# Kernel tuning notes

Hardware: AMD Instinct MI355X
Metric: run time of the kernel (lower is better)

Reference implementation:

```python
import jax, jax.numpy as jnp
import numpy as np

PATCH = 768
POS = 64
HID = 512
B, N = 8, 2048


def setup_inputs() -> dict:
    key = jax.random.key(0)
    ks = jax.random.split(key, 8)
    d_in = PATCH + POS
    s = 1.0 / np.sqrt(d_in)
    return {
        "patches": jax.random.normal(ks[0], (B, N, PATCH), jnp.float32),
        "positions": jax.random.normal(ks[1], (B, N, POS), jnp.float32),
        "Wq": jax.random.uniform(ks[2], (d_in, HID), jnp.float32, -s, s),
        "bq": jax.random.uniform(ks[3], (HID,), jnp.float32, -s, s),
        "Wk": jax.random.uniform(ks[4], (d_in, HID), jnp.float32, -s, s),
        "bk": jax.random.uniform(ks[5], (d_in and HID,), jnp.float32, -s, s),
        "Wv": jax.random.uniform(ks[6], (d_in, HID), jnp.float32, -s, s),
        "bv": jax.random.uniform(ks[7], (HID,), jnp.float32, -s, s),
    }


def reference(patches, positions, Wq, bq, Wk, bk, Wv, bv):
    # concat patch features with positional features: [B, N, PATCH+POS]
    x = jnp.concatenate([patches, positions], axis=-1)
    Q = x @ Wq + bq  # [B, N, HID]
    K = x @ Wk + bk
    V = x @ Wv + bv
    scale = jnp.sqrt(jnp.asarray(HID, x.dtype))
    scores = jnp.einsum("bnd,bmd->bnm", Q, K) / scale  # [B, N, N]
    weights = jax.nn.softmax(scores, axis=-1)
    return jnp.einsum("bnm,bmd->bnd", weights, V)  # [B, N, HID]
```

## Files before the change

kernel.cpp:

```cpp
#include <hip/hip_runtime.h>
#include <hip/hip_bf16.h>
#include <math.h>

typedef __hip_bfloat16 bf16;
typedef __attribute__((ext_vector_type(4))) float f32x4;
typedef __attribute__((ext_vector_type(8))) short s16x8;

typedef const __attribute__((address_space(1))) void gvoid_t;
typedef __attribute__((address_space(3))) void lvoid_t;

__device__ __forceinline__ void gload16(const void* g, void* l) {
  __builtin_amdgcn_global_load_lds((gvoid_t*)g, (lvoid_t*)l, 16, 0, 0);
}
__device__ __forceinline__ unsigned short f2b(float f) {
  bf16 h = __float2bfloat16(f);
  return *(unsigned short*)&h;
}

__global__ __launch_bounds__(256) void prep_x(const float* __restrict__ patches,
                                              const float* __restrict__ positions,
                                              bf16* __restrict__ xb) {
  const long long row = blockIdx.x;
  const int c = threadIdx.x;
  const bool lo = (c < 192);
  const bool hi = (c >= 192) && (c < 208);
  const float* src = lo ? (patches + row * 768 + c * 4)
                        : (positions + row * 64 + (c - 192) * 4);
  if (lo || hi) {
    float4 v = *(const float4*)src;
    const int dst = lo ? (c * 4) : (768 + (c - 192) * 4);
    uint2 w;
    w.x = (unsigned int)f2b(v.x) | ((unsigned int)f2b(v.y) << 16);
    w.y = (unsigned int)f2b(v.z) | ((unsigned int)f2b(v.w) << 16);
    *(uint2*)(xb + row * 832 + dst) = w;
  }
}

__global__ __launch_bounds__(256) void prep_w(const float* __restrict__ Wq,
                                              const float* __restrict__ Wk,
                                              const float* __restrict__ Wv,
                                              bf16* __restrict__ Wt) {
  __shared__ float tile[32][33];
  const int z = blockIdx.z;
  const float* W = (z == 0) ? Wq : (z == 1) ? Wk : Wv;
  bf16* T = Wt + (long long)z * 512 * 832;
  const int n0 = blockIdx.x * 32;
  const int k0 = blockIdx.y * 32;
  const int tx = threadIdx.x, ty = threadIdx.y;
  #pragma unroll
  for (int i = 0; i < 32; i += 8)
    tile[ty + i][tx] = W[(long long)(k0 + ty + i) * 512 + n0 + tx];
  __syncthreads();
  #pragma unroll
  for (int i = 0; i < 32; i += 8)
    T[(long long)(n0 + ty + i) * 832 + k0 + tx] = __float2bfloat16(tile[tx][ty + i]);
}

__global__ __launch_bounds__(256) void gemm_qkv(
    const bf16* __restrict__ xb, const bf16* __restrict__ Wt,
    const float* __restrict__ bq, const float* __restrict__ bk,
    const float* __restrict__ bv,
    bf16* __restrict__ qk, bf16* __restrict__ vt) {
  __shared__ bf16 As[128 * 64];
  __shared__ bf16 Bs[128 * 64];
  const int tid = threadIdx.x;
  const int wave = tid >> 6, lane = tid & 63;
  const int llo = lane & 15, lhi = lane >> 4;
  const int wm = wave >> 1, wn = wave & 1;

  const unsigned int lin = blockIdx.x;
  const unsigned int xcd = lin & 7u, idx = lin >> 3;
  const unsigned int g = xcd * 192u + idx;
  const unsigned int bm_t = g / 12u;
  const unsigned int bn_t = g - bm_t * 12u;
  const int row0 = (int)bm_t * 128;
  const int col0 = (int)bn_t * 128;
  const int z = col0 >> 9;

  f32x4 acc[4][4] = {};

  for (int kt = 0; kt < 832; kt += 64) {
    #pragma unroll
    for (int i = 0; i < 4; i++) {
      const int c = i * 256 + tid;
      const int r = c >> 3, cc = c & 7;
      const int kk = (cc ^ (r & 7)) << 3;
      gload16(xb + ((long long)(row0 + r) * 832 + kt + kk),
              (char*)As + (long long)(i * 256 + wave * 64) * 16);
      gload16(Wt + ((long long)(col0 + r) * 832 + kt + kk),
              (char*)Bs + (long long)(i * 256 + wave * 64) * 16);
    }
    __syncthreads();
    #pragma unroll
    for (int k0 = 0; k0 < 64; k0 += 32) {
      const int xk = ((((k0 >> 3) + lhi) ^ (llo & 7)) << 3);
      s16x8 af[4], bfr[4];
      #pragma unroll
      for (int mf = 0; mf < 4; mf++)
        af[mf] = *(const s16x8*)&As[(wm * 64 + mf * 16 + llo) * 64 + xk];
      #pragma unroll
      for (int nf = 0; nf < 4; nf++)
        bfr[nf] = *(const s16x8*)&Bs[(wn * 64 + nf * 16 + llo) * 64 + xk];
      #pragma unroll
      for (int mf = 0; mf < 4; mf++)
        #pragma unroll
        for (int nf = 0; nf < 4; nf++)
          acc[mf][nf] = __builtin_amdgcn_mfma_f32_16x16x32_bf16(
              af[mf], bfr[nf], acc[mf][nf], 0, 0, 0);
    }
    __syncthreads();
  }

  if (z < 2) {
    const float* bias = z ? bk : bq;
    bf16* outp = qk + (long long)z * 16384 * 512;
    #pragma unroll
    for (int mf = 0; mf < 4; mf++)
      #pragma unroll
      for (int nf = 0; nf < 4; nf++) {
        const int c = (col0 & 511) + wn * 64 + nf * 16 + llo;
        const int grow0 = row0 + wm * 64 + mf * 16 + lhi * 4;
        const float bb = bias[c];
        #pragma unroll
        for (int r = 0; r < 4; r++)
          outp[(long long)(grow0 + r) * 512 + c] =
              __float2bfloat16(acc[mf][nf][r] + bb);
      }
  } else {
    #pragma unroll
    for (int mf = 0; mf < 4; mf++)
      #pragma unroll
      for (int nf = 0; nf < 4; nf++) {
        const int c = (col0 & 511) + wn * 64 + nf * 16 + llo;
        const int grow0 = row0 + wm * 64 + mf * 16 + lhi * 4;
        const int b = grow0 >> 11, j = grow0 & 2047;
        const float bb = bv[c];
        uint2 w;
        w.x = (unsigned int)f2b(acc[mf][nf][0] + bb) |
              ((unsigned int)f2b(acc[mf][nf][1] + bb) << 16);
        w.y = (unsigned int)f2b(acc[mf][nf][2] + bb) |
              ((unsigned int)f2b(acc[mf][nf][3] + bb) << 16);
        *(uint2*)(vt + (long long)b * 512 * 2048 + (long long)c * 2048 + j) = w;
      }
  }
}

__global__ __launch_bounds__(256) void gemm_scores(const bf16* __restrict__ qk,
                                                   bf16* __restrict__ S,
                                                   float* __restrict__ rowsum) {
  __shared__ bf16 As[128 * 64];
  __shared__ bf16 Bs[128 * 64];
  const int tid = threadIdx.x;
  const int wave = tid >> 6, lane = tid & 63;
  const int llo = lane & 15, lhi = lane >> 4;
  const int wm = wave >> 1, wn = wave & 1;

  const unsigned int lin = blockIdx.x;
  const unsigned int xcd = lin & 7u, idx = lin >> 3;
  const unsigned int g = xcd * 256u + idx;
  const int b = (int)(g >> 8);
  const unsigned int rem = g & 255u;
  const int row0 = (int)(rem >> 4) * 128;
  const int col0 = (int)(rem & 15u) * 128;

  const bf16* Ab = qk + (long long)b * 2048 * 512;
  const bf16* Bb = qk + (long long)16384 * 512 + (long long)b * 2048 * 512;

  f32x4 acc[4][4] = {};
  for (int kt = 0; kt < 512; kt += 64) {
    #pragma unroll
    for (int i = 0; i < 4; i++) {
      const int c = i * 256 + tid;
      const int r = c >> 3, cc = c & 7;
      const int kk = (cc ^ (r & 7)) << 3;
      gload16(Ab + ((long long)(row0 + r) * 512 + kt + kk),
              (char*)As + (long long)(i * 256 + wave * 64) * 16);
      gload16(Bb + ((long long)(col0 + r) * 512 + kt + kk),
              (char*)Bs + (long long)(i * 256 + wave * 64) * 16);
    }
    __syncthreads();
    #pragma unroll
    for (int k0 = 0; k0 < 64; k0 += 32) {
      const int xk = ((((k0 >> 3) + lhi) ^ (llo & 7)) << 3);
      s16x8 af[4], bfr[4];
      #pragma unroll
      for (int mf = 0; mf < 4; mf++)
        af[mf] = *(const s16x8*)&As[(wm * 64 + mf * 16 + llo) * 64 + xk];
      #pragma unroll
      for (int nf = 0; nf < 4; nf++)
        bfr[nf] = *(const s16x8*)&Bs[(wn * 64 + nf * 16 + llo) * 64 + xk];
      #pragma unroll
      for (int mf = 0; mf < 4; mf++)
        #pragma unroll
        for (int nf = 0; nf < 4; nf++)
          acc[mf][nf] = __builtin_amdgcn_mfma_f32_16x16x32_bf16(
              af[mf], bfr[nf], acc[mf][nf], 0, 0, 0);
    }
    __syncthreads();
  }

  const float alpha = 0.044194173824159216f;
  #pragma unroll
  for (int mf = 0; mf < 4; mf++)
    #pragma unroll
    for (int nf = 0; nf < 4; nf++)
      #pragma unroll
      for (int r = 0; r < 4; r++)
        acc[mf][nf][r] = __expf(acc[mf][nf][r] * alpha);

  bf16* Sb = S + (long long)b * 2048 * 2048;
  #pragma unroll
  for (int mf = 0; mf < 4; mf++)
    #pragma unroll
    for (int nf = 0; nf < 4; nf++) {
      const int gcol = col0 + wn * 64 + nf * 16 + llo;
      const int grow0 = row0 + wm * 64 + mf * 16 + lhi * 4;
      #pragma unroll
      for (int r = 0; r < 4; r++)
        Sb[(long long)(grow0 + r) * 2048 + gcol] =
            __float2bfloat16(acc[mf][nf][r]);
    }

  float* rs = rowsum + (long long)b * 2048;
  #pragma unroll
  for (int mf = 0; mf < 4; mf++) {
    #pragma unroll
    for (int r = 0; r < 4; r++) {
      float p = acc[mf][0][r] + acc[mf][1][r] + acc[mf][2][r] + acc[mf][3][r];
      p += __shfl_xor(p, 1, 64);
      p += __shfl_xor(p, 2, 64);
      p += __shfl_xor(p, 4, 64);
      p += __shfl_xor(p, 8, 64);
      if (llo == 0)
        atomicAdd(&rs[row0 + wm * 64 + mf * 16 + lhi * 4 + r], p);
    }
  }
}

__global__ __launch_bounds__(256) void gemm_pv(const bf16* __restrict__ S,
                                               const bf16* __restrict__ vt,
                                               const float* __restrict__ rowsum,
                                               float* __restrict__ out) {
  __shared__ bf16 As[64 * 64];
  __shared__ bf16 Bs[128 * 64];
  const int tid = threadIdx.x;
  const int wave = tid >> 6, lane = tid & 63;
  const int llo = lane & 15, lhi = lane >> 4;
  const int wm = wave >> 1, wn = wave & 1;

  const unsigned int lin = blockIdx.x;
  const unsigned int xcd = lin & 7u, idx = lin >> 3;
  const int b = (int)xcd;
  const int row0 = (int)(idx >> 2) * 64;
  const int col0 = (int)(idx & 3u) * 128;

  const bf16* Ab = S + (long long)b * 2048 * 2048;
  const bf16* Bb = vt + (long long)b * 512 * 2048;

  f32x4 acc[2][4] = {};
  for (int kt = 0; kt < 2048; kt += 64) {
    #pragma unroll
    for (int i = 0; i < 2; i++) {
      const int c = i * 256 + tid;
      const int r = c >> 3, cc = c & 7;
      const int kk = (cc ^ (r & 7)) << 3;
      gload16(Ab + ((long long)(row0 + r) * 2048 + kt + kk),
              (char*)As + (long long)(i * 256 + wave * 64) * 16);
    }
    #pragma unroll
    for (int i = 0; i < 4; i++) {
      const int c = i * 256 + tid;
      const int r = c >> 3, cc = c & 7;
      const int kk = (cc ^ (r & 7)) << 3;
      gload16(Bb + ((long long)(col0 + r) * 2048 + kt + kk),
              (char*)Bs + (long long)(i * 256 + wave * 64) * 16);
    }
    __syncthreads();
    #pragma unroll
    for (int k0 = 0; k0 < 64; k0 += 32) {
      const int xk = ((((k0 >> 3) + lhi) ^ (llo & 7)) << 3);
      s16x8 af[2], bfr[4];
      #pragma unroll
      for (int mf = 0; mf < 2; mf++)
        af[mf] = *(const s16x8*)&As[(wm * 32 + mf * 16 + llo) * 64 + xk];
      #pragma unroll
      for (int nf = 0; nf < 4; nf++)
        bfr[nf] = *(const s16x8*)&Bs[(wn * 64 + nf * 16 + llo) * 64 + xk];
      #pragma unroll
      for (int mf = 0; mf < 2; mf++)
        #pragma unroll
        for (int nf = 0; nf < 4; nf++)
          acc[mf][nf] = __builtin_amdgcn_mfma_f32_16x16x32_bf16(
              af[mf], bfr[nf], acc[mf][nf], 0, 0, 0);
    }
    __syncthreads();
  }

  const float* rs = rowsum + (long long)b * 2048;
  float* Ob = out + (long long)b * 2048 * 512;
  #pragma unroll
  for (int mf = 0; mf < 2; mf++) {
    const int grow0 = row0 + wm * 32 + mf * 16 + lhi * 4;
    float inv[4];
    #pragma unroll
    for (int r = 0; r < 4; r++) inv[r] = 1.0f / rs[grow0 + r];
    #pragma unroll
    for (int nf = 0; nf < 4; nf++) {
      const int gcol = col0 + wn * 64 + nf * 16 + llo;
      #pragma unroll
      for (int r = 0; r < 4; r++)
        Ob[(long long)(grow0 + r) * 512 + gcol] = acc[mf][nf][r] * inv[r];
    }
  }
}

extern "C" void kernel_launch(void* const* d_in, const int* in_sizes, int n_in,
                              void* d_out, int out_size, void* d_ws, size_t ws_size,
                              hipStream_t stream) {
  const float* patches = (const float*)d_in[0];
  const float* positions = (const float*)d_in[1];
  const float* Wq = (const float*)d_in[2];
  const float* bq = (const float*)d_in[3];
  const float* Wk = (const float*)d_in[4];
  const float* bk = (const float*)d_in[5];
  const float* Wv = (const float*)d_in[6];
  const float* bv = (const float*)d_in[7];
  float* out = (float*)d_out;

  if (ws_size < 147324928u) return;

  char* ws = (char*)d_ws;
  bf16* Wt = (bf16*)(ws);
  bf16* xb = (bf16*)(ws + 2555904);
  bf16* qk = (bf16*)(ws + 29818880);
  bf16* vt = (bf16*)(ws + 63373312);
  bf16* S  = (bf16*)(ws + 80150528);
  float* rowsum = (float*)(ws + 147259392);

  hipMemsetAsync(rowsum, 0, 16384 * sizeof(float), stream);
  prep_x<<<16384, 256, 0, stream>>>(patches, positions, xb);
  prep_w<<<dim3(16, 26, 3), dim3(32, 8), 0, stream>>>(Wq, Wk, Wv, Wt);
  gemm_qkv<<<1536, 256, 0, stream>>>(xb, Wt, bq, bk, bv, qk, vt);
  gemm_scores<<<2048, 256, 0, stream>>>(qk, S, rowsum);
  gemm_pv<<<1024, 256, 0, stream>>>(S, vt, rowsum, out);
}
```

Measured before the change: 287.8 us.

## Replace rowsum atomics with partial sums and enlarge PV tile to 128x128

The scores kernel now reduces row sums within the block through shared memory and writes per-column-tile partials instead of issuing global atomicAdds. A new small kernel sums the partials and stores reciprocals, which also removes the memset. The PV GEMM tile grows from 64x128 to 128x128, so each S row and V tile is loaded from global memory fewer times. The trade-offs are an extra kernel launch, a larger accumulator register footprint, and half as many PV blocks, which may lower occupancy.

```diff
diff --git a/kernel.cpp b/kernel.cpp
--- a/kernel.cpp
+++ b/kernel.cpp
@@ -147,9 +147,10 @@
 
 __global__ __launch_bounds__(256) void gemm_scores(const bf16* __restrict__ qk,
                                                    bf16* __restrict__ S,
-                                                   float* __restrict__ rowsum) {
+                                                   float* __restrict__ rowsumP) {
   __shared__ bf16 As[128 * 64];
   __shared__ bf16 Bs[128 * 64];
+  __shared__ float psum[4][64];
   const int tid = threadIdx.x;
   const int wave = tid >> 6, lane = tid & 63;
   const int llo = lane & 15, lhi = lane >> 4;
@@ -161,7 +162,8 @@
   const int b = (int)(g >> 8);
   const unsigned int rem = g & 255u;
   const int row0 = (int)(rem >> 4) * 128;
-  const int col0 = (int)(rem & 15u) * 128;
+  const int coltile = (int)(rem & 15u);
+  const int col0 = coltile * 128;
 
   const bf16* Ab = qk + (long long)b * 2048 * 512;
   const bf16* Bb = qk + (long long)16384 * 512 + (long long)b * 2048 * 512;
@@ -221,7 +223,6 @@
             __float2bfloat16(acc[mf][nf][r]);
     }
 
-  float* rs = rowsum + (long long)b * 2048;
   #pragma unroll
   for (int mf = 0; mf < 4; mf++) {
     #pragma unroll
@@ -231,17 +232,33 @@
       p += __shfl_xor(p, 2, 64);
       p += __shfl_xor(p, 4, 64);
       p += __shfl_xor(p, 8, 64);
-      if (llo == 0)
-        atomicAdd(&rs[row0 + wm * 64 + mf * 16 + lhi * 4 + r], p);
-    }
-  }
+      if (llo == 0) psum[wave][mf * 16 + lhi * 4 + r] = p;
+    }
+  }
+  __syncthreads();
+  if (tid < 128) {
+    const int wmx = tid >> 6, i = tid & 63;
+    const float v = psum[wmx * 2][i] + psum[wmx * 2 + 1][i];
+    rowsumP[((long long)(b * 16 + coltile)) * 2048 + row0 + wmx * 64 + i] = v;
+  }
+}
+
+__global__ __launch_bounds__(256) void reduce_rowsum(
+    const float* __restrict__ rowsumP, float* __restrict__ rinv) {
+  const int i = blockIdx.x * 256 + threadIdx.x;
+  const int b = i >> 11, row = i & 2047;
+  const float* p = rowsumP + ((long long)b * 16) * 2048 + row;
+  float s = 0.f;
+  #pragma unroll
+  for (int t = 0; t < 16; t++) s += p[t * 2048];
+  rinv[i] = 1.0f / s;
 }
 
 __global__ __launch_bounds__(256) void gemm_pv(const bf16* __restrict__ S,
                                                const bf16* __restrict__ vt,
-                                               const float* __restrict__ rowsum,
+                                               const float* __restrict__ rinv,
                                                float* __restrict__ out) {
-  __shared__ bf16 As[64 * 64];
+  __shared__ bf16 As[128 * 64];
   __shared__ bf16 Bs[128 * 64];
   const int tid = threadIdx.x;
   const int wave = tid >> 6, lane = tid & 63;
@@ -251,27 +268,21 @@
   const unsigned int lin = blockIdx.x;
   const unsigned int xcd = lin & 7u, idx = lin >> 3;
   const int b = (int)xcd;
-  const int row0 = (int)(idx >> 2) * 64;
+  const int row0 = (int)(idx >> 2) * 128;
   const int col0 = (int)(idx & 3u) * 128;
 
   const bf16* Ab = S + (long long)b * 2048 * 2048;
   const bf16* Bb = vt + (long long)b * 512 * 2048;
 
-  f32x4 acc[2][4] = {};
+  f32x4 acc[4][4] = {};
   for (int kt = 0; kt < 2048; kt += 64) {
     #pragma unroll
-    for (int i = 0; i < 2; i++) {
+    for (int i = 0; i < 4; i++) {
       const int c = i * 256 + tid;
       const int r = c >> 3, cc = c & 7;
       const int kk = (cc ^ (r & 7)) << 3;
       gload16(Ab + ((long long)(row0 + r) * 2048 + kt + kk),
               (char*)As + (long long)(i * 256 + wave * 64) * 16);
-    }
-    #pragma unroll
-    for (int i = 0; i < 4; i++) {
-      const int c = i * 256 + tid;
-      const int r = c >> 3, cc = c & 7;
-      const int kk = (cc ^ (r & 7)) << 3;
       gload16(Bb + ((long long)(col0 + r) * 2048 + kt + kk),
               (char*)Bs + (long long)(i * 256 + wave * 64) * 16);
     }
@@ -279,15 +290,15 @@
     #pragma unroll
     for (int k0 = 0; k0 < 64; k0 += 32) {
       const int xk = ((((k0 >> 3) + lhi) ^ (llo & 7)) << 3);
-      s16x8 af[2], bfr[4];
-      #pragma unroll
-      for (int mf = 0; mf < 2; mf++)
-        af[mf] = *(const s16x8*)&As[(wm * 32 + mf * 16 + llo) * 64 + xk];
+      s16x8 af[4], bfr[4];
+      #pragma unroll
+      for (int mf = 0; mf < 4; mf++)
+        af[mf] = *(const s16x8*)&As[(wm * 64 + mf * 16 + llo) * 64 + xk];
       #pragma unroll
       for (int nf = 0; nf < 4; nf++)
         bfr[nf] = *(const s16x8*)&Bs[(wn * 64 + nf * 16 + llo) * 64 + xk];
       #pragma unroll
-      for (int mf = 0; mf < 2; mf++)
+      for (int mf = 0; mf < 4; mf++)
         #pragma unroll
         for (int nf = 0; nf < 4; nf++)
           acc[mf][nf] = __builtin_amdgcn_mfma_f32_16x16x32_bf16(
@@ -296,20 +307,20 @@
     __syncthreads();
   }
 
-  const float* rs = rowsum + (long long)b * 2048;
+  const float* rs = rinv + (long long)b * 2048;
   float* Ob = out + (long long)b * 2048 * 512;
   #pragma unroll
-  for (int mf = 0; mf < 2; mf++) {
-    const int grow0 = row0 + wm * 32 + mf * 16 + lhi * 4;
-    float inv[4];
-    #pragma unroll
-    for (int r = 0; r < 4; r++) inv[r] = 1.0f / rs[grow0 + r];
+  for (int mf = 0; mf < 4; mf++) {
+    const int grow0 = row0 + wm * 64 + mf * 16 + lhi * 4;
+    float iv[4];
+    #pragma unroll
+    for (int r = 0; r < 4; r++) iv[r] = rs[grow0 + r];
     #pragma unroll
     for (int nf = 0; nf < 4; nf++) {
       const int gcol = col0 + wn * 64 + nf * 16 + llo;
       #pragma unroll
       for (int r = 0; r < 4; r++)
-        Ob[(long long)(grow0 + r) * 512 + gcol] = acc[mf][nf][r] * inv[r];
+        Ob[(long long)(grow0 + r) * 512 + gcol] = acc[mf][nf][r] * iv[r];
     }
   }
 }
@@ -327,7 +338,7 @@
   const float* bv = (const float*)d_in[7];
   float* out = (float*)d_out;
 
-  if (ws_size < 147324928u) return;
+  if (ws_size < 149422080u) return;
 
   char* ws = (char*)d_ws;
   bf16* Wt = (bf16*)(ws);
@@ -335,12 +346,13 @@
   bf16* qk = (bf16*)(ws + 29818880);
   bf16* vt = (bf16*)(ws + 63373312);
   bf16* S  = (bf16*)(ws + 80150528);
-  float* rowsum = (float*)(ws + 147259392);
-
-  hipMemsetAsync(rowsum, 0, 16384 * sizeof(float), stream);
+  float* rinv    = (float*)(ws + 147259392);
+  float* rowsumP = (float*)(ws + 147324928);
+
   prep_x<<<16384, 256, 0, stream>>>(patches, positions, xb);
   prep_w<<<dim3(16, 26, 3), dim3(32, 8), 0, stream>>>(Wq, Wk, Wv, Wt);
   gemm_qkv<<<1536, 256, 0, stream>>>(xb, Wt, bq, bk, bv, qk, vt);
-  gemm_scores<<<2048, 256, 0, stream>>>(qk, S, rowsum);
-  gemm_pv<<<1024, 256, 0, stream>>>(S, vt, rowsum, out);
-}
+  gemm_scores<<<2048, 256, 0, stream>>>(qk, S, rowsumP);
+  reduce_rowsum<<<64, 256, 0, stream>>>(rowsumP, rinv);
+  gemm_pv<<<512, 256, 0, stream>>>(S, vt, rinv, out);
+}
```

Result: faster. 274.6 us (-4.6%).
